# Performance work log

Measured on AMD Instinct MI355X. Metric: run time of the kernel, lower is better.

Reference implementation:

```python
import jax, jax.numpy as jnp
import numpy as np

N = 100000   # num nodes
E = 3200000  # num edges (avg degree 32)
EPS = 1e-5   # BatchNorm eps


def _gcn_norm(edge_index, edge_weight, n):
    # add self loops with weight 1 (PyG gcn_norm default fill_value=1.0)
    loops = jnp.arange(n, dtype=edge_index.dtype)
    ei = jnp.concatenate([edge_index, jnp.stack([loops, loops])], axis=1)
    ew = jnp.concatenate([edge_weight, jnp.ones((n,), edge_weight.dtype)])
    row, col = ei[0], ei[1]
    deg = jax.ops.segment_sum(ew, col, num_segments=n)
    deg_safe = jnp.where(deg > 0, deg, 1.0)
    dinv = jnp.where(deg > 0, jax.lax.rsqrt(deg_safe), 0.0)
    norm = dinv[row] * ew * dinv[col]  # [E+N]
    return row, col, norm


def _gcn_conv(x, row, col, norm, W, b, n):
    h = x @ W                                   # [N, out]
    msg = h[row] * norm[:, None]                # gather + scale, [E+N, out]
    out = jax.ops.segment_sum(msg, col, num_segments=n)  # scatter-add
    return out + b


def _bn(x, g, b, rm, rv):
    # BatchNorm1d in eval mode: running statistics
    return (x - rm) * jax.lax.rsqrt(rv + EPS) * g + b


def setup_inputs() -> dict:
    key = jax.random.key(0)
    ks = jax.random.split(key, 24)
    def p(i, shape, scale=1.0):
        return jax.random.normal(ks[i], shape, dtype=jnp.float32) * scale
    inp = {
        "x": p(0, (N, 1)),
        "edge_index": jax.random.randint(ks[1], (2, E), 0, N, dtype=jnp.int32),
        "edge_weight": jax.random.uniform(ks[2], (E,), dtype=jnp.float32),
        # GCNConv weights (glorot-ish scale) and biases
        "W1": p(3, (1, 16), 0.5), "b1": jnp.zeros((16,), jnp.float32),
        "W2": p(4, (16, 4), 0.25), "b2": jnp.zeros((4,), jnp.float32),
        "W3": p(5, (4, 1), 0.5), "b3": jnp.zeros((1,), jnp.float32),
        # BatchNorm params + running stats (running_var > 0)
        "g1": p(6, (16,), 0.1) + 1.0, "be1": p(7, (16,), 0.1),
        "rm1": p(8, (16,), 0.1), "rv1": jax.random.uniform(ks[9], (16,)) + 0.5,
        "g2": p(10, (4,), 0.1) + 1.0, "be2": p(11, (4,), 0.1),
        "rm2": p(12, (4,), 0.1), "rv2": jax.random.uniform(ks[13], (4,)) + 0.5,
        "g3": p(14, (1,), 0.1) + 1.0, "be3": p(15, (1,), 0.1),
        "rm3": p(16, (1,), 0.1), "rv3": jax.random.uniform(ks[17], (1,)) + 0.5,
        # end Linear(1, 1)
        "Wl": p(18, (1, 1)), "bl": p(19, (1,), 0.1),
    }
    return inp


def reference(x, edge_index, edge_weight,
              W1, b1, W2, b2, W3, b3,
              g1, be1, rm1, rv1,
              g2, be2, rm2, rv2,
              g3, be3, rm3, rv3,
              Wl, bl):
    row, col, norm = _gcn_norm(edge_index, edge_weight, N)
    h = _gcn_conv(x, row, col, norm, W1, b1, N)
    h = jax.nn.relu(_bn(h, g1, be1, rm1, rv1))  # dropout = identity in eval
    h = _gcn_conv(h, row, col, norm, W2, b2, N)
    h = jax.nn.relu(_bn(h, g2, be2, rm2, rv2))
    h = _gcn_conv(h, row, col, norm, W3, b3, N)
    h = _bn(h, g3, be3, rm3, rv3)
    h = h @ Wl + bl
    return jax.nn.sigmoid(h)
```

## Files before the change

### kernel.cpp

```cpp
#include <hip/hip_runtime.h>
#include <math.h>

#define NN 100000
#define NE 3200000
#define EPSBN 1e-5f

#define BSH 7
#define NB 782
#define NBLK 500
#define CHUNK 6400
#define C4 (CHUNK/4)
#define CAP 5120
#define BTA 512

#define NSB 12512
#define STCAP 4608

__device__ __forceinline__ float wave_allreduce(float a) {
    a += __shfl_xor(a, 1);  a += __shfl_xor(a, 2);  a += __shfl_xor(a, 4);
    a += __shfl_xor(a, 8);  a += __shfl_xor(a, 16); a += __shfl_xor(a, 32);
    return a;
}

__global__ void k_params_zero(const float* __restrict__ W1, const float* __restrict__ b1,
                              const float* __restrict__ g1, const float* __restrict__ be1,
                              const float* __restrict__ rm1, const float* __restrict__ rv1,
                              const float* __restrict__ b2,
                              const float* __restrict__ g2, const float* __restrict__ be2,
                              const float* __restrict__ rm2, const float* __restrict__ rv2,
                              const float* __restrict__ b3,
                              const float* __restrict__ g3, const float* __restrict__ be3,
                              const float* __restrict__ rm3, const float* __restrict__ rv3,
                              const float* __restrict__ Wl, const float* __restrict__ bl,
                              float* __restrict__ P, int* __restrict__ cnt) {
    int f = threadIdx.x;
    for (int i = f; i < NB; i += 1024) cnt[i] = 0;
    if (f < 16) {
        float k = g1[f] * rsqrtf(rv1[f] + EPSBN);
        P[f]      = W1[f] * k;
        P[16 + f] = (b1[f] - rm1[f]) * k + be1[f];
    }
    if (f < 4) {
        float k = g2[f] * rsqrtf(rv2[f] + EPSBN);
        P[32 + f] = k;
        P[36 + f] = (b2[f] - rm2[f]) * k + be2[f];
    }
    if (f == 0) {
        float k = g3[0] * rsqrtf(rv3[0] + EPSBN);
        P[40] = k * Wl[0];
        P[41] = ((b3[0] - rm3[0]) * k + be3[0]) * Wl[0] + bl[0];
    }
}

__global__ void k_build(const int* __restrict__ row, const int* __restrict__ col,
                        const float* __restrict__ ew, int* __restrict__ cnt,
                        uint2* __restrict__ rec) {
    __shared__ int h[NB];
    __shared__ int gb[NB];
    __shared__ int gsum[98];
    __shared__ uint2 st[CHUNK];
    __shared__ unsigned short sb[CHUNK];
    int blk = blockIdx.x, tid = threadIdx.x;
    for (int j = tid; j < NB; j += BTA) h[j] = 0;
    __syncthreads();

    const int4* c4 = (const int4*)(col + blk * CHUNK);
    int rk[4][4];
#pragma unroll
    for (int it = 0; it < 4; ++it) {
        int i = tid + it * BTA;
        if (i < C4) {
            int4 c = c4[i];
            rk[it][0] = atomicAdd(&h[c.x >> BSH], 1);
            rk[it][1] = atomicAdd(&h[c.y >> BSH], 1);
            rk[it][2] = atomicAdd(&h[c.z >> BSH], 1);
            rk[it][3] = atomicAdd(&h[c.w >> BSH], 1);
        }
    }
    __syncthreads();

    for (int j = tid; j < NB; j += BTA) {
        int hj = h[j];
        gb[j] = hj ? atomicAdd(&cnt[j], hj) : 0;
    }

    if (tid < 98) {
        int s = 0, b0 = tid * 8;
#pragma unroll
        for (int k = 0; k < 8; ++k) { int idx = b0 + k; s += (idx < NB) ? h[idx] : 0; }
        gsum[tid] = s;
    }
    __syncthreads();
    if (tid == 0) {
        int run = 0;
        for (int g = 0; g < 98; ++g) { int t = gsum[g]; gsum[g] = run; run += t; }
    }
    __syncthreads();
    if (tid < 98) {
        int run = gsum[tid], b0 = tid * 8;
#pragma unroll
        for (int k = 0; k < 8; ++k) {
            int idx = b0 + k;
            if (idx < NB) { int t = h[idx]; h[idx] = run; run += t; }
        }
    }
    __syncthreads();

    const int4*   r4 = (const int4*)(row + blk * CHUNK);
    const float4* w4 = (const float4*)(ew + blk * CHUNK);
#pragma unroll
    for (int it = 0; it < 4; ++it) {
        int i = tid + it * BTA;
        if (i < C4) {
            int4 c = c4[i]; int4 r = r4[i]; float4 w = w4[i];
            int b0 = c.x >> BSH, b1 = c.y >> BSH, b2 = c.z >> BSH, b3 = c.w >> BSH;
            int s0 = h[b0] + rk[it][0];
            st[s0] = make_uint2((unsigned)r.x | ((unsigned)(c.x & 127) << 17), __float_as_uint(w.x));
            sb[s0] = (unsigned short)b0;
            int s1 = h[b1] + rk[it][1];
            st[s1] = make_uint2((unsigned)r.y | ((unsigned)(c.y & 127) << 17), __float_as_uint(w.y));
            sb[s1] = (unsigned short)b1;
            int s2 = h[b2] + rk[it][2];
            st[s2] = make_uint2((unsigned)r.z | ((unsigned)(c.z & 127) << 17), __float_as_uint(w.z));
            sb[s2] = (unsigned short)b2;
            int s3 = h[b3] + rk[it][3];
            st[s3] = make_uint2((unsigned)r.w | ((unsigned)(c.w & 127) << 17), __float_as_uint(w.w));
            sb[s3] = (unsigned short)b3;
        }
    }
    __syncthreads();

    for (int i = tid; i < CHUNK; i += BTA) {
        int b = sb[i];
        rec[(size_t)b * CAP + gb[b] + (i - h[b])] = st[i];
    }
}

__global__ void k_subsort_deg(const int* __restrict__ cnt, uint2* __restrict__ rec,
                              int2* __restrict__ subsn, const float* __restrict__ x,
                              float* __restrict__ dinv, float* __restrict__ xd) {
    __shared__ uint2 st[STCAP];
    __shared__ int subtot[16];
    __shared__ int live[16];
    __shared__ int sstart[16];
    __shared__ int scount[16];
    int bin = blockIdx.x, tid = threadIdx.x;
    int lane = tid & 63, wv = tid >> 6;
    int n = cnt[bin];
    if (n > STCAP) n = STCAP;
    uint2* rb = rec + (size_t)bin * CAP;
    for (int i = tid; i < n; i += BTA) st[i] = rb[i];
    if (tid < 16) subtot[tid] = 0;
    __syncthreads();

    int myCnt = 0;
    for (int base = tid - lane; base < n; base += BTA) {
        int i = base + lane;
        bool v = (i < n);
        unsigned key = v ? ((st[i].x >> 20) & 15u) : 0u;
        unsigned long long bv = __ballot(v);
        unsigned long long q0 = __ballot(key & 1u);
        unsigned long long q1 = __ballot(key & 2u);
        unsigned long long q2 = __ballot(key & 4u);
        unsigned long long q3 = __ballot(key & 8u);
        if (lane < 16) {
            unsigned k = (unsigned)lane;
            unsigned long long m = bv;
            m &= (k & 1u) ? q0 : ~q0;
            m &= (k & 2u) ? q1 : ~q1;
            m &= (k & 4u) ? q2 : ~q2;
            m &= (k & 8u) ? q3 : ~q3;
            myCnt += __popcll(m);
        }
    }
    if (lane < 16 && myCnt) atomicAdd(&subtot[lane], myCnt);
    __syncthreads();

    if (tid == 0) {
        int run = 0;
        for (int k = 0; k < 16; ++k) {
            live[k] = run; sstart[k] = run; scount[k] = subtot[k];
            subsn[bin * 16 + k] = make_int2(bin * CAP + run, subtot[k]);
            run += subtot[k];
        }
    }
    __syncthreads();

    for (int base = tid - lane; base < n; base += BTA) {
        int i = base + lane;
        bool v = (i < n);
        uint2 rcd = v ? st[i] : make_uint2(0u, 0u);
        unsigned key = v ? ((rcd.x >> 20) & 15u) : 0u;
        unsigned long long bv = __ballot(v);
        unsigned long long q0 = __ballot(key & 1u);
        unsigned long long q1 = __ballot(key & 2u);
        unsigned long long q2 = __ballot(key & 4u);
        unsigned long long q3 = __ballot(key & 8u);
        int gb = 0;
        if (lane < 16) {
            unsigned k = (unsigned)lane;
            unsigned long long m = bv;
            m &= (k & 1u) ? q0 : ~q0;
            m &= (k & 2u) ? q1 : ~q1;
            m &= (k & 4u) ? q2 : ~q2;
            m &= (k & 8u) ? q3 : ~q3;
            int c = __popcll(m);
            if (c) gb = atomicAdd(&live[(int)k], c);
        }
        unsigned long long same = bv;
        same &= (key & 1u) ? q0 : ~q0;
        same &= (key & 2u) ? q1 : ~q1;
        same &= (key & 4u) ? q2 : ~q2;
        same &= (key & 8u) ? q3 : ~q3;
        unsigned long long below = (lane == 0) ? 0ull : ((~0ull) >> (64 - lane));
        int rank = __popcll(same & below);
        int mybase = __shfl(gb, (int)key);
        if (v) rb[mybase + rank] = rcd;
    }
    __syncthreads();

    for (int s = 0; s < 2; ++s) {
        int sbx = (wv << 1) | s;
        int n0 = scount[sbx];
        const uint2* p = rb + sstart[sbx];
        float acc[8] = {0.f, 0.f, 0.f, 0.f, 0.f, 0.f, 0.f, 0.f};
        for (int i = lane; i < n0; i += 64) {
            uint2 v = p[i];
            int cl = (v.x >> 17) & 7;
            float w = __uint_as_float(v.y);
#pragma unroll
            for (int c = 0; c < 8; ++c) acc[c] += (cl == c) ? w : 0.f;
        }
#pragma unroll
        for (int c = 0; c < 8; ++c) acc[c] = wave_allreduce(acc[c]);
        float mine = acc[0];
#pragma unroll
        for (int c = 1; c < 8; ++c) mine = (lane == c) ? acc[c] : mine;
        int colv = (bin << BSH) + (sbx << 3) + lane;
        if (lane < 8 && colv < NN) {
            float d = rsqrtf(1.0f + mine);
            dinv[colv] = d;
            xd[colv] = x[colv] * d;
        }
    }
}


__global__ void k_agg1_2(const int2* __restrict__ subsn, const uint2* __restrict__ rec,
                         const float* __restrict__ dinv, const float* __restrict__ xd,
                         const float* __restrict__ P, const float* __restrict__ W2,
                         float* __restrict__ m2s) {
    int tid = threadIdx.x, lane = tid & 63, wv = tid >> 6;
    int b = blockIdx.x * 8 + wv;
    int2 sn = subsn[b];
    float acc[8] = {0.f, 0.f, 0.f, 0.f, 0.f, 0.f, 0.f, 0.f};
    const uint2* p = rec + sn.x;
    int n0 = sn.y;
    int i = lane;
    for (; i + 64 < n0; i += 128) {
        uint2 v0 = p[i], v1 = p[i + 64];
        float g0 = xd[v0.x & 0x1FFFF] * __uint_as_float(v0.y);
        float g1 = xd[v1.x & 0x1FFFF] * __uint_as_float(v1.y);
        int c0 = (v0.x >> 17) & 7, c1 = (v1.x >> 17) & 7;
#pragma unroll
        for (int c = 0; c < 8; ++c) {
            acc[c] += (c0 == c) ? g0 : 0.f;
            acc[c] += (c1 == c) ? g1 : 0.f;
        }
    }
    for (; i < n0; i += 64) {
        uint2 v = p[i];
        int cl = (v.x >> 17) & 7;
        float g = xd[v.x & 0x1FFFF] * __uint_as_float(v.y);
#pragma unroll
        for (int c = 0; c < 8; ++c) acc[c] += (cl == c) ? g : 0.f;
    }
#pragma unroll
    for (int c = 0; c < 8; ++c) acc[c] = wave_allreduce(acc[c]);
    float mine = acc[0];
#pragma unroll
    for (int c = 1; c < 8; ++c) mine = (lane == c) ? acc[c] : mine;
    int colv = b * 8 + lane;
    if (lane < 8 && colv < NN) {
        float dc = dinv[colv];
        float y = (mine + xd[colv]) * dc;
        float m0 = 0.f, m1 = 0.f, m2v = 0.f, m3v = 0.f;
#pragma unroll
        for (int f = 0; f < 16; ++f) {
            float z = fmaxf(fmaf(y, P[f], P[16 + f]), 0.0f);
            m0 = fmaf(z, W2[f * 4 + 0], m0);
            m1 = fmaf(z, W2[f * 4 + 1], m1);
            m2v = fmaf(z, W2[f * 4 + 2], m2v);
            m3v = fmaf(z, W2[f * 4 + 3], m3v);
        }
        *(float4*)(m2s + 4 * colv) = make_float4(m0 * dc, m1 * dc, m2v * dc, m3v * dc);
    }
}

__global__ void k_agg2_2(const int2* __restrict__ subsn, const uint2* __restrict__ rec,
                         const float* __restrict__ dinv, const float* __restrict__ m2s,
                         const float* __restrict__ P, const float* __restrict__ W3,
                         float* __restrict__ m3s) {
    int tid = threadIdx.x, lane = tid & 63, wv = tid >> 6;
    int b = blockIdx.x * 8 + wv;
    int2 sn = subsn[b];
    float acc[8][4];
#pragma unroll
    for (int c = 0; c < 8; ++c)
#pragma unroll
        for (int j = 0; j < 4; ++j) acc[c][j] = 0.f;
    const uint2* p = rec + sn.x;
    int n0 = sn.y;
    int i = lane;
    for (; i + 64 < n0; i += 128) {
        uint2 v0 = p[i], v1 = p[i + 64];
        float w0 = __uint_as_float(v0.y), w1 = __uint_as_float(v1.y);
        float4 ma = *(const float4*)(m2s + 4 * (v0.x & 0x1FFFF));
        float4 mb = *(const float4*)(m2s + 4 * (v1.x & 0x1FFFF));
        int c0 = (v0.x >> 17) & 7, c1 = (v1.x >> 17) & 7;
#pragma unroll
        for (int c = 0; c < 8; ++c) {
            float s0 = (c0 == c) ? w0 : 0.f;
            float s1 = (c1 == c) ? w1 : 0.f;
            acc[c][0] = fmaf(ma.x, s0, fmaf(mb.x, s1, acc[c][0]));
            acc[c][1] = fmaf(ma.y, s0, fmaf(mb.y, s1, acc[c][1]));
            acc[c][2] = fmaf(ma.z, s0, fmaf(mb.z, s1, acc[c][2]));
            acc[c][3] = fmaf(ma.w, s0, fmaf(mb.w, s1, acc[c][3]));
        }
    }
    for (; i < n0; i += 64) {
        uint2 v = p[i];
        int cl = (v.x >> 17) & 7;
        float w = __uint_as_float(v.y);
        float4 m = *(const float4*)(m2s + 4 * (v.x & 0x1FFFF));
#pragma unroll
        for (int c = 0; c < 8; ++c) {
            float sel = (cl == c) ? w : 0.f;
            acc[c][0] = fmaf(m.x, sel, acc[c][0]);
            acc[c][1] = fmaf(m.y, sel, acc[c][1]);
            acc[c][2] = fmaf(m.z, sel, acc[c][2]);
            acc[c][3] = fmaf(m.w, sel, acc[c][3]);
        }
    }
#pragma unroll
    for (int c = 0; c < 8; ++c)
#pragma unroll
        for (int j = 0; j < 4; ++j) acc[c][j] = wave_allreduce(acc[c][j]);
    float r0 = acc[0][0], r1 = acc[0][1], r2 = acc[0][2], r3 = acc[0][3];
#pragma unroll
    for (int c = 1; c < 8; ++c) {
        r0 = (lane == c) ? acc[c][0] : r0;
        r1 = (lane == c) ? acc[c][1] : r1;
        r2 = (lane == c) ? acc[c][2] : r2;
        r3 = (lane == c) ? acc[c][3] : r3;
    }
    int colv = b * 8 + lane;
    if (lane < 8 && colv < NN) {
        float dc = dinv[colv];
        float4 mc = *(const float4*)(m2s + 4 * colv);
        float a0 = (r0 + mc.x) * dc;
        float a1 = (r1 + mc.y) * dc;
        float a2 = (r2 + mc.z) * dc;
        float a3 = (r3 + mc.w) * dc;
        float v3 = 0.f;
        v3 = fmaf(fmaxf(fmaf(a0, P[32], P[36]), 0.f), W3[0], v3);
        v3 = fmaf(fmaxf(fmaf(a1, P[33], P[37]), 0.f), W3[1], v3);
        v3 = fmaf(fmaxf(fmaf(a2, P[34], P[38]), 0.f), W3[2], v3);
        v3 = fmaf(fmaxf(fmaf(a3, P[35], P[39]), 0.f), W3[3], v3);
        m3s[colv] = v3 * dc;
    }
}

__global__ void k_agg3_2(const int2* __restrict__ subsn, const uint2* __restrict__ rec,
                         const float* __restrict__ dinv, const float* __restrict__ m3s,
                         const float* __restrict__ P, float* __restrict__ out) {
    int tid = threadIdx.x, lane = tid & 63, wv = tid >> 6;
    int b = blockIdx.x * 8 + wv;
    int2 sn = subsn[b];
    float acc[8] = {0.f, 0.f, 0.f, 0.f, 0.f, 0.f, 0.f, 0.f};
    const uint2* p = rec + sn.x;
    int n0 = sn.y;
    int i = lane;
    for (; i + 64 < n0; i += 128) {
        uint2 v0 = p[i], v1 = p[i + 64];
        float g0 = m3s[v0.x & 0x1FFFF] * __uint_as_float(v0.y);
        float g1 = m3s[v1.x & 0x1FFFF] * __uint_as_float(v1.y);
        int c0 = (v0.x >> 17) & 7, c1 = (v1.x >> 17) & 7;
#pragma unroll
        for (int c = 0; c < 8; ++c) {
            acc[c] += (c0 == c) ? g0 : 0.f;
            acc[c] += (c1 == c) ? g1 : 0.f;
        }
    }
    for (; i < n0; i += 64) {
        uint2 v = p[i];
        int cl = (v.x >> 17) & 7;
        float g = m3s[v.x & 0x1FFFF] * __uint_as_float(v.y);
#pragma unroll
        for (int c = 0; c < 8; ++c) acc[c] += (cl == c) ? g : 0.f;
    }
#pragma unroll
    for (int c = 0; c < 8; ++c) acc[c] = wave_allreduce(acc[c]);
    float mine = acc[0];
#pragma unroll
    for (int c = 1; c < 8; ++c) mine = (lane == c) ? acc[c] : mine;
    int colv = b * 8 + lane;
    if (lane < 8 && colv < NN) {
        float t = fmaf((mine + m3s[colv]) * dinv[colv], P[40], P[41]);
        out[colv] = 1.0f / (1.0f + __expf(-t));
    }
}


__global__ void k_init_deg(float* __restrict__ deg) {
    int i = blockIdx.x * blockDim.x + threadIdx.x;
    if (i < NN) deg[i] = 1.0f;
}

__global__ void k_dinv_y1(const float* __restrict__ deg, const float* __restrict__ x,
                          float* __restrict__ dinv, float* __restrict__ y1) {
    int i = blockIdx.x * blockDim.x + threadIdx.x;
    if (i >= NN) return;
    float d = rsqrtf(deg[i]);
    dinv[i] = d;
    y1[i] = x[i] * d * d;
}

__global__ void k_l1_epi(const float* __restrict__ y1, const float* __restrict__ dinv,
                         const float* __restrict__ P, const float* __restrict__ W2,
                         float* __restrict__ m2, float* __restrict__ agg2) {
    int i = blockIdx.x * blockDim.x + threadIdx.x;
    if (i >= NN) return;
    float y = y1[i];
    float m0 = 0.f, m1 = 0.f, m2v = 0.f, m3v = 0.f;
#pragma unroll
    for (int f = 0; f < 16; ++f) {
        float z = fmaxf(fmaf(y, P[f], P[16 + f]), 0.0f);
        m0 = fmaf(z, W2[f * 4 + 0], m0);
        m1 = fmaf(z, W2[f * 4 + 1], m1);
        m2v = fmaf(z, W2[f * 4 + 2], m2v);
        m3v = fmaf(z, W2[f * 4 + 3], m3v);
    }
    float d = dinv[i];
    float d2 = d * d;
    *(float4*)(m2 + 4 * i)   = make_float4(m0, m1, m2v, m3v);
    *(float4*)(agg2 + 4 * i) = make_float4(m0 * d2, m1 * d2, m2v * d2, m3v * d2);
}

__global__ void k_l2_epi(const float* __restrict__ agg2, const float* __restrict__ dinv,
                         const float* __restrict__ P, const float* __restrict__ W3,
                         float* __restrict__ m3, float* __restrict__ agg3) {
    int i = blockIdx.x * blockDim.x + threadIdx.x;
    if (i >= NN) return;
    float4 a = *(const float4*)(agg2 + 4 * i);
    float v = 0.f;
    v = fmaf(fmaxf(fmaf(a.x, P[32], P[36]), 0.f), W3[0], v);
    v = fmaf(fmaxf(fmaf(a.y, P[33], P[37]), 0.f), W3[1], v);
    v = fmaf(fmaxf(fmaf(a.z, P[34], P[38]), 0.f), W3[2], v);
    v = fmaf(fmaxf(fmaf(a.w, P[35], P[39]), 0.f), W3[3], v);
    float d = dinv[i];
    m3[i] = v;
    agg3[i] = v * d * d;
}

__global__ void k_final(const float* __restrict__ agg3, const float* __restrict__ P,
                        float* __restrict__ out) {
    int i = blockIdx.x * blockDim.x + threadIdx.x;
    if (i >= NN) return;
    float t = fmaf(agg3[i], P[40], P[41]);
    out[i] = 1.0f / (1.0f + __expf(-t));
}

__global__ void k_deg(const int* __restrict__ col, const float* __restrict__ ew,
                      float* __restrict__ deg) {
    int e = (blockIdx.x * blockDim.x + threadIdx.x) * 4;
    if (e >= NE) return;
    int4 c = *(const int4*)(col + e);
    float4 w = *(const float4*)(ew + e);
    atomicAdd(&deg[c.x], w.x);
    atomicAdd(&deg[c.y], w.y);
    atomicAdd(&deg[c.z], w.z);
    atomicAdd(&deg[c.w], w.w);
}

__global__ void k_norm_agg1(const int* __restrict__ row, const int* __restrict__ col,
                            const float* __restrict__ ew, const float* __restrict__ dinv,
                            const float* __restrict__ x,
                            float* __restrict__ norm, float* __restrict__ y1) {
    int e = (blockIdx.x * blockDim.x + threadIdx.x) * 4;
    if (e >= NE) return;
    int4 r = *(const int4*)(row + e);
    int4 c = *(const int4*)(col + e);
    float4 w = *(const float4*)(ew + e);
    float4 nv;
    nv.x = dinv[r.x] * w.x * dinv[c.x];
    nv.y = dinv[r.y] * w.y * dinv[c.y];
    nv.z = dinv[r.z] * w.z * dinv[c.z];
    nv.w = dinv[r.w] * w.w * dinv[c.w];
    *(float4*)(norm + e) = nv;
    atomicAdd(&y1[c.x], x[r.x] * nv.x);
    atomicAdd(&y1[c.y], x[r.y] * nv.y);
    atomicAdd(&y1[c.z], x[r.z] * nv.z);
    atomicAdd(&y1[c.w], x[r.w] * nv.w);
}

__global__ void k_agg2(const int* __restrict__ row, const int* __restrict__ col,
                       const float* __restrict__ norm, const float* __restrict__ m2,
                       float* __restrict__ agg2) {
    int e = blockIdx.x * blockDim.x + threadIdx.x;
    if (e >= NE) return;
    int r = row[e], c = col[e];
    float nv = norm[e];
    float4 m = *(const float4*)(m2 + 4 * r);
    atomicAdd(&agg2[4 * c + 0], m.x * nv);
    atomicAdd(&agg2[4 * c + 1], m.y * nv);
    atomicAdd(&agg2[4 * c + 2], m.z * nv);
    atomicAdd(&agg2[4 * c + 3], m.w * nv);
}

__global__ void k_agg3(const int* __restrict__ row, const int* __restrict__ col,
                       const float* __restrict__ norm, const float* __restrict__ m3,
                       float* __restrict__ agg3) {
    int e = (blockIdx.x * blockDim.x + threadIdx.x) * 4;
    if (e >= NE) return;
    int4 r = *(const int4*)(row + e);
    int4 c = *(const int4*)(col + e);
    float4 nv = *(const float4*)(norm + e);
    atomicAdd(&agg3[c.x], m3[r.x] * nv.x);
    atomicAdd(&agg3[c.y], m3[r.y] * nv.y);
    atomicAdd(&agg3[c.z], m3[r.z] * nv.z);
    atomicAdd(&agg3[c.w], m3[r.w] * nv.w);
}


extern "C" void kernel_launch(void* const* d_in, const int* in_sizes, int n_in,
                              void* d_out, int out_size, void* d_ws, size_t ws_size,
                              hipStream_t stream) {
    const float* x  = (const float*)d_in[0];
    const int*   ei = (const int*)d_in[1];
    const float* ew = (const float*)d_in[2];
    const float* W1 = (const float*)d_in[3];
    const float* b1 = (const float*)d_in[4];
    const float* W2 = (const float*)d_in[5];
    const float* b2 = (const float*)d_in[6];
    const float* W3 = (const float*)d_in[7];
    const float* b3 = (const float*)d_in[8];
    const float* g1 = (const float*)d_in[9];
    const float* be1 = (const float*)d_in[10];
    const float* rm1 = (const float*)d_in[11];
    const float* rv1 = (const float*)d_in[12];
    const float* g2 = (const float*)d_in[13];
    const float* be2 = (const float*)d_in[14];
    const float* rm2 = (const float*)d_in[15];
    const float* rv2 = (const float*)d_in[16];
    const float* g3 = (const float*)d_in[17];
    const float* be3 = (const float*)d_in[18];
    const float* rm3 = (const float*)d_in[19];
    const float* rv3 = (const float*)d_in[20];
    const float* Wl = (const float*)d_in[21];
    const float* bl = (const float*)d_in[22];
    float* out = (float*)d_out;

    const int* row = ei;
    const int* col = ei + NE;

    const int BT = 256;
    const int gN = (NN + BT - 1) / BT;
    const int gE4 = (NE / 4 + BT - 1) / BT;

    char* ws = (char*)d_ws;

    if (ws_size >= 37000000u) {
        float* P     = (float*)(ws);
        int*   cnt   = (int*)  (ws + 4096);
        int2*  subsn = (int2*) (ws + 16384);
        float* dinv  = (float*)(ws + 524288);
        float* xd    = (float*)(ws + 1048576);
        float* m3s   = (float*)(ws + 1572864);
        float* m2s   = (float*)(ws + 2097152);
        uint2* rec   = (uint2*)(ws + 4194304);

        k_params_zero<<<1, 1024, 0, stream>>>(W1, b1, g1, be1, rm1, rv1,
                                              b2, g2, be2, rm2, rv2,
                                              b3, g3, be3, rm3, rv3, Wl, bl, P, cnt);
        k_build<<<NBLK, BTA, 0, stream>>>(row, col, ew, cnt, rec);
        k_subsort_deg<<<NB, BTA, 0, stream>>>(cnt, rec, subsn, x, dinv, xd);
        k_agg1_2<<<NSB / 8, BTA, 0, stream>>>(subsn, rec, dinv, xd, P, W2, m2s);
        k_agg2_2<<<NSB / 8, BTA, 0, stream>>>(subsn, rec, dinv, m2s, P, W3, m3s);
        k_agg3_2<<<NSB / 8, BTA, 0, stream>>>(subsn, rec, dinv, m3s, P, out);
    } else {
        float* deg   = (float*)(ws);
        float* dinv  = (float*)(ws + 400000);
        float* y1    = (float*)(ws + 800000);
        float* m2    = (float*)(ws + 1200000);
        float* agg2  = (float*)(ws + 2800000);
        float* m3    = (float*)(ws + 4400000);
        float* agg3  = (float*)(ws + 4800000);
        float* Pf    = (float*)(ws + 5200000);
        float* norm  = (float*)(ws + 5200256);
        const int gE1 = (NE + BT - 1) / BT;

        k_params_zero<<<1, 1024, 0, stream>>>(W1, b1, g1, be1, rm1, rv1,
                                              b2, g2, be2, rm2, rv2,
                                              b3, g3, be3, rm3, rv3, Wl, bl, Pf, (int*)(ws + 5300000));
        k_init_deg<<<gN, BT, 0, stream>>>(deg);
        k_deg<<<gE4, BT, 0, stream>>>(col, ew, deg);
        k_dinv_y1<<<gN, BT, 0, stream>>>(deg, x, dinv, y1);
        k_norm_agg1<<<gE4, BT, 0, stream>>>(row, col, ew, dinv, x, norm, y1);
        k_l1_epi<<<gN, BT, 0, stream>>>(y1, dinv, Pf, W2, m2, agg2);
        k_agg2<<<gE1, BT, 0, stream>>>(row, col, norm, m2, agg2);
        k_l2_epi<<<gN, BT, 0, stream>>>(agg2, dinv, Pf, W3, m3, agg3);
        k_agg3<<<gE4, BT, 0, stream>>>(row, col, norm, m3, agg3);
        k_final<<<gN, BT, 0, stream>>>(agg3, Pf, out);
    }
}
```

Before: 134.6 us.

## Fully sort edges by column and aggregate with one thread per column

The subsort kernel now sorts records by the full 7-bit in-bin column key, staging records in registers and writing the sorted order through shared memory. It emits a per-column start/count table. The three aggregation kernels switch from wave-per-8-columns with select-accumulate and wave allreduces to one thread per column looping over its contiguous edge segment. This removes redundant select ALU work and shuffle reductions, at the cost of uncoalesced per-thread record reads and possible load imbalance across columns.

```diff
diff --git a/kernel.cpp b/kernel.cpp
--- a/kernel.cpp
+++ b/kernel.cpp
@@ -13,8 +13,8 @@
 #define CAP 5120
 #define BTA 512
 
-#define NSB 12512
 #define STCAP 4608
+#define NCOL 100096
 
 __device__ __forceinline__ float wave_allreduce(float a) {
     a += __shfl_xor(a, 1);  a += __shfl_xor(a, 2);  a += __shfl_xor(a, 4);
@@ -137,11 +137,12 @@
 }
 
 __global__ void k_subsort_deg(const int* __restrict__ cnt, uint2* __restrict__ rec,
-                              int2* __restrict__ subsn, const float* __restrict__ x,
+                              int2* __restrict__ colsc, const float* __restrict__ x,
                               float* __restrict__ dinv, float* __restrict__ xd) {
     __shared__ uint2 st[STCAP];
-    __shared__ int subtot[16];
-    __shared__ int live[16];
+    __shared__ int subtot[128];
+    __shared__ int colbase[128];
+    __shared__ int live[128];
     __shared__ int sstart[16];
     __shared__ int scount[16];
     int bin = blockIdx.x, tid = threadIdx.x;
@@ -149,80 +150,109 @@
     int n = cnt[bin];
     if (n > STCAP) n = STCAP;
     uint2* rb = rec + (size_t)bin * CAP;
-    for (int i = tid; i < n; i += BTA) st[i] = rb[i];
-    if (tid < 16) subtot[tid] = 0;
-    __syncthreads();
-
-    int myCnt = 0;
-    for (int base = tid - lane; base < n; base += BTA) {
-        int i = base + lane;
+
+    uint2 r[9];
+#pragma unroll
+    for (int k = 0; k < 9; ++k) {
+        int i = tid + k * BTA;
+        if (i < n) r[k] = rb[i];
+    }
+    if (tid < 128) subtot[tid] = 0;
+    __syncthreads();
+
+    int c0acc = 0, c1acc = 0;
+#pragma unroll
+    for (int k = 0; k < 9; ++k) {
+        int i = tid + k * BTA;
         bool v = (i < n);
-        unsigned key = v ? ((st[i].x >> 20) & 15u) : 0u;
+        unsigned key = v ? ((r[k].x >> 17) & 127u) : 0u;
         unsigned long long bv = __ballot(v);
         unsigned long long q0 = __ballot(key & 1u);
         unsigned long long q1 = __ballot(key & 2u);
         unsigned long long q2 = __ballot(key & 4u);
         unsigned long long q3 = __ballot(key & 8u);
-        if (lane < 16) {
-            unsigned k = (unsigned)lane;
-            unsigned long long m = bv;
-            m &= (k & 1u) ? q0 : ~q0;
-            m &= (k & 2u) ? q1 : ~q1;
-            m &= (k & 4u) ? q2 : ~q2;
-            m &= (k & 8u) ? q3 : ~q3;
-            myCnt += __popcll(m);
-        }
-    }
-    if (lane < 16 && myCnt) atomicAdd(&subtot[lane], myCnt);
+        unsigned long long q4 = __ballot(key & 16u);
+        unsigned long long q5 = __ballot(key & 32u);
+        unsigned long long q6 = __ballot(key & 64u);
+        unsigned long long m5 = bv;
+        m5 &= (lane & 1)  ? q0 : ~q0;
+        m5 &= (lane & 2)  ? q1 : ~q1;
+        m5 &= (lane & 4)  ? q2 : ~q2;
+        m5 &= (lane & 8)  ? q3 : ~q3;
+        m5 &= (lane & 16) ? q4 : ~q4;
+        m5 &= (lane & 32) ? q5 : ~q5;
+        c0acc += __popcll(m5 & ~q6);
+        c1acc += __popcll(m5 & q6);
+    }
+    if (c0acc) atomicAdd(&subtot[lane], c0acc);
+    if (c1acc) atomicAdd(&subtot[lane + 64], c1acc);
     __syncthreads();
 
     if (tid == 0) {
         int run = 0;
-        for (int k = 0; k < 16; ++k) {
-            live[k] = run; sstart[k] = run; scount[k] = subtot[k];
-            subsn[bin * 16 + k] = make_int2(bin * CAP + run, subtot[k]);
+        for (int k = 0; k < 128; ++k) {
+            colbase[k] = run; live[k] = run;
             run += subtot[k];
         }
-    }
-    __syncthreads();
-
-    for (int base = tid - lane; base < n; base += BTA) {
-        int i = base + lane;
+        for (int s = 0; s < 16; ++s) {
+            sstart[s] = colbase[s * 8];
+            int e = (s == 15) ? n : colbase[s * 8 + 8];
+            scount[s] = e - sstart[s];
+        }
+    }
+    __syncthreads();
+
+    if (tid < 128)
+        colsc[bin * 128 + tid] = make_int2(bin * CAP + colbase[tid], subtot[tid]);
+
+#pragma unroll
+    for (int k = 0; k < 9; ++k) {
+        int i = tid + k * BTA;
         bool v = (i < n);
-        uint2 rcd = v ? st[i] : make_uint2(0u, 0u);
-        unsigned key = v ? ((rcd.x >> 20) & 15u) : 0u;
+        uint2 rcd = v ? r[k] : make_uint2(0u, 0u);
+        unsigned key = v ? ((rcd.x >> 17) & 127u) : 0u;
         unsigned long long bv = __ballot(v);
         unsigned long long q0 = __ballot(key & 1u);
         unsigned long long q1 = __ballot(key & 2u);
         unsigned long long q2 = __ballot(key & 4u);
         unsigned long long q3 = __ballot(key & 8u);
-        int gb = 0;
-        if (lane < 16) {
-            unsigned k = (unsigned)lane;
-            unsigned long long m = bv;
-            m &= (k & 1u) ? q0 : ~q0;
-            m &= (k & 2u) ? q1 : ~q1;
-            m &= (k & 4u) ? q2 : ~q2;
-            m &= (k & 8u) ? q3 : ~q3;
-            int c = __popcll(m);
-            if (c) gb = atomicAdd(&live[(int)k], c);
-        }
+        unsigned long long q4 = __ballot(key & 16u);
+        unsigned long long q5 = __ballot(key & 32u);
+        unsigned long long q6 = __ballot(key & 64u);
+        unsigned long long m5 = bv;
+        m5 &= (lane & 1)  ? q0 : ~q0;
+        m5 &= (lane & 2)  ? q1 : ~q1;
+        m5 &= (lane & 4)  ? q2 : ~q2;
+        m5 &= (lane & 8)  ? q3 : ~q3;
+        m5 &= (lane & 16) ? q4 : ~q4;
+        m5 &= (lane & 32) ? q5 : ~q5;
+        int cc0 = __popcll(m5 & ~q6);
+        int cc1 = __popcll(m5 & q6);
+        int gb0 = cc0 ? atomicAdd(&live[lane], cc0) : 0;
+        int gb1 = cc1 ? atomicAdd(&live[lane + 64], cc1) : 0;
         unsigned long long same = bv;
-        same &= (key & 1u) ? q0 : ~q0;
-        same &= (key & 2u) ? q1 : ~q1;
-        same &= (key & 4u) ? q2 : ~q2;
-        same &= (key & 8u) ? q3 : ~q3;
+        same &= (key & 1u)  ? q0 : ~q0;
+        same &= (key & 2u)  ? q1 : ~q1;
+        same &= (key & 4u)  ? q2 : ~q2;
+        same &= (key & 8u)  ? q3 : ~q3;
+        same &= (key & 16u) ? q4 : ~q4;
+        same &= (key & 32u) ? q5 : ~q5;
+        same &= (key & 64u) ? q6 : ~q6;
         unsigned long long below = (lane == 0) ? 0ull : ((~0ull) >> (64 - lane));
         int rank = __popcll(same & below);
-        int mybase = __shfl(gb, (int)key);
-        if (v) rb[mybase + rank] = rcd;
-    }
-    __syncthreads();
+        int s0 = __shfl(gb0, (int)(key & 63u));
+        int s1 = __shfl(gb1, (int)(key & 63u));
+        int mybase = (key & 64u) ? s1 : s0;
+        if (v) st[mybase + rank] = rcd;
+    }
+    __syncthreads();
+
+    for (int i = tid; i < n; i += BTA) rb[i] = st[i];
 
     for (int s = 0; s < 2; ++s) {
         int sbx = (wv << 1) | s;
         int n0 = scount[sbx];
-        const uint2* p = rb + sstart[sbx];
+        const uint2* p = &st[sstart[sbx]];
         float acc[8] = {0.f, 0.f, 0.f, 0.f, 0.f, 0.f, 0.f, 0.f};
         for (int i = lane; i < n0; i += 64) {
             uint2 v = p[i];
@@ -246,169 +276,98 @@
 }
 
 
-__global__ void k_agg1_2(const int2* __restrict__ subsn, const uint2* __restrict__ rec,
+__global__ void k_agg1_c(const int2* __restrict__ colsc, const uint2* __restrict__ rec,
                          const float* __restrict__ dinv, const float* __restrict__ xd,
                          const float* __restrict__ P, const float* __restrict__ W2,
                          float* __restrict__ m2s) {
-    int tid = threadIdx.x, lane = tid & 63, wv = tid >> 6;
-    int b = blockIdx.x * 8 + wv;
-    int2 sn = subsn[b];
-    float acc[8] = {0.f, 0.f, 0.f, 0.f, 0.f, 0.f, 0.f, 0.f};
-    const uint2* p = rec + sn.x;
-    int n0 = sn.y;
-    int i = lane;
-    for (; i + 64 < n0; i += 128) {
-        uint2 v0 = p[i], v1 = p[i + 64];
+    int col = blockIdx.x * blockDim.x + threadIdx.x;
+    if (col >= NN) return;
+    int2 sc = colsc[col];
+    const uint2* p = rec + sc.x;
+    float a = 0.f;
+    int i = 0;
+    for (; i + 1 < sc.y; i += 2) {
+        uint2 v0 = p[i], v1 = p[i + 1];
         float g0 = xd[v0.x & 0x1FFFF] * __uint_as_float(v0.y);
         float g1 = xd[v1.x & 0x1FFFF] * __uint_as_float(v1.y);
-        int c0 = (v0.x >> 17) & 7, c1 = (v1.x >> 17) & 7;
-#pragma unroll
-        for (int c = 0; c < 8; ++c) {
-            acc[c] += (c0 == c) ? g0 : 0.f;
-            acc[c] += (c1 == c) ? g1 : 0.f;
-        }
-    }
-    for (; i < n0; i += 64) {
-        uint2 v = p[i];
-        int cl = (v.x >> 17) & 7;
-        float g = xd[v.x & 0x1FFFF] * __uint_as_float(v.y);
-#pragma unroll
-        for (int c = 0; c < 8; ++c) acc[c] += (cl == c) ? g : 0.f;
-    }
-#pragma unroll
-    for (int c = 0; c < 8; ++c) acc[c] = wave_allreduce(acc[c]);
-    float mine = acc[0];
-#pragma unroll
-    for (int c = 1; c < 8; ++c) mine = (lane == c) ? acc[c] : mine;
-    int colv = b * 8 + lane;
-    if (lane < 8 && colv < NN) {
-        float dc = dinv[colv];
-        float y = (mine + xd[colv]) * dc;
-        float m0 = 0.f, m1 = 0.f, m2v = 0.f, m3v = 0.f;
-#pragma unroll
-        for (int f = 0; f < 16; ++f) {
-            float z = fmaxf(fmaf(y, P[f], P[16 + f]), 0.0f);
-            m0 = fmaf(z, W2[f * 4 + 0], m0);
-            m1 = fmaf(z, W2[f * 4 + 1], m1);
-            m2v = fmaf(z, W2[f * 4 + 2], m2v);
-            m3v = fmaf(z, W2[f * 4 + 3], m3v);
-        }
-        *(float4*)(m2s + 4 * colv) = make_float4(m0 * dc, m1 * dc, m2v * dc, m3v * dc);
-    }
-}
-
-__global__ void k_agg2_2(const int2* __restrict__ subsn, const uint2* __restrict__ rec,
+        a += g0 + g1;
+    }
+    if (i < sc.y) { uint2 v = p[i]; a += xd[v.x & 0x1FFFF] * __uint_as_float(v.y); }
+    float dc = dinv[col];
+    float y = (a + xd[col]) * dc;
+    float m0 = 0.f, m1 = 0.f, m2v = 0.f, m3v = 0.f;
+#pragma unroll
+    for (int f = 0; f < 16; ++f) {
+        float z = fmaxf(fmaf(y, P[f], P[16 + f]), 0.0f);
+        m0 = fmaf(z, W2[f * 4 + 0], m0);
+        m1 = fmaf(z, W2[f * 4 + 1], m1);
+        m2v = fmaf(z, W2[f * 4 + 2], m2v);
+        m3v = fmaf(z, W2[f * 4 + 3], m3v);
+    }
+    *(float4*)(m2s + 4 * col) = make_float4(m0 * dc, m1 * dc, m2v * dc, m3v * dc);
+}
+
+__global__ void k_agg2_c(const int2* __restrict__ colsc, const uint2* __restrict__ rec,
                          const float* __restrict__ dinv, const float* __restrict__ m2s,
                          const float* __restrict__ P, const float* __restrict__ W3,
                          float* __restrict__ m3s) {
-    int tid = threadIdx.x, lane = tid & 63, wv = tid >> 6;
-    int b = blockIdx.x * 8 + wv;
-    int2 sn = subsn[b];
-    float acc[8][4];
-#pragma unroll
-    for (int c = 0; c < 8; ++c)
-#pragma unroll
-        for (int j = 0; j < 4; ++j) acc[c][j] = 0.f;
-    const uint2* p = rec + sn.x;
-    int n0 = sn.y;
-    int i = lane;
-    for (; i + 64 < n0; i += 128) {
-        uint2 v0 = p[i], v1 = p[i + 64];
+    int col = blockIdx.x * blockDim.x + threadIdx.x;
+    if (col >= NN) return;
+    int2 sc = colsc[col];
+    const uint2* p = rec + sc.x;
+    float a0 = 0.f, a1 = 0.f, a2 = 0.f, a3 = 0.f;
+    int i = 0;
+    for (; i + 1 < sc.y; i += 2) {
+        uint2 v0 = p[i], v1 = p[i + 1];
         float w0 = __uint_as_float(v0.y), w1 = __uint_as_float(v1.y);
         float4 ma = *(const float4*)(m2s + 4 * (v0.x & 0x1FFFF));
         float4 mb = *(const float4*)(m2s + 4 * (v1.x & 0x1FFFF));
-        int c0 = (v0.x >> 17) & 7, c1 = (v1.x >> 17) & 7;
-#pragma unroll
-        for (int c = 0; c < 8; ++c) {
-            float s0 = (c0 == c) ? w0 : 0.f;
-            float s1 = (c1 == c) ? w1 : 0.f;
-            acc[c][0] = fmaf(ma.x, s0, fmaf(mb.x, s1, acc[c][0]));
-            acc[c][1] = fmaf(ma.y, s0, fmaf(mb.y, s1, acc[c][1]));
-            acc[c][2] = fmaf(ma.z, s0, fmaf(mb.z, s1, acc[c][2]));
-            acc[c][3] = fmaf(ma.w, s0, fmaf(mb.w, s1, acc[c][3]));
-        }
-    }
-    for (; i < n0; i += 64) {
+        a0 = fmaf(ma.x, w0, fmaf(mb.x, w1, a0));
+        a1 = fmaf(ma.y, w0, fmaf(mb.y, w1, a1));
+        a2 = fmaf(ma.z, w0, fmaf(mb.z, w1, a2));
+        a3 = fmaf(ma.w, w0, fmaf(mb.w, w1, a3));
+    }
+    if (i < sc.y) {
         uint2 v = p[i];
-        int cl = (v.x >> 17) & 7;
         float w = __uint_as_float(v.y);
         float4 m = *(const float4*)(m2s + 4 * (v.x & 0x1FFFF));
-#pragma unroll
-        for (int c = 0; c < 8; ++c) {
-            float sel = (cl == c) ? w : 0.f;
-            acc[c][0] = fmaf(m.x, sel, acc[c][0]);
-            acc[c][1] = fmaf(m.y, sel, acc[c][1]);
-            acc[c][2] = fmaf(m.z, sel, acc[c][2]);
-            acc[c][3] = fmaf(m.w, sel, acc[c][3]);
-        }
-    }
-#pragma unroll
-    for (int c = 0; c < 8; ++c)
-#pragma unroll
-        for (int j = 0; j < 4; ++j) acc[c][j] = wave_allreduce(acc[c][j]);
-    float r0 = acc[0][0], r1 = acc[0][1], r2 = acc[0][2], r3 = acc[0][3];
-#pragma unroll
-    for (int c = 1; c < 8; ++c) {
-        r0 = (lane == c) ? acc[c][0] : r0;
-        r1 = (lane == c) ? acc[c][1] : r1;
-        r2 = (lane == c) ? acc[c][2] : r2;
-        r3 = (lane == c) ? acc[c][3] : r3;
-    }
-    int colv = b * 8 + lane;
-    if (lane < 8 && colv < NN) {
-        float dc = dinv[colv];
-        float4 mc = *(const float4*)(m2s + 4 * colv);
-        float a0 = (r0 + mc.x) * dc;
-        float a1 = (r1 + mc.y) * dc;
-        float a2 = (r2 + mc.z) * dc;
-        float a3 = (r3 + mc.w) * dc;
-        float v3 = 0.f;
-        v3 = fmaf(fmaxf(fmaf(a0, P[32], P[36]), 0.f), W3[0], v3);
-        v3 = fmaf(fmaxf(fmaf(a1, P[33], P[37]), 0.f), W3[1], v3);
-        v3 = fmaf(fmaxf(fmaf(a2, P[34], P[38]), 0.f), W3[2], v3);
-        v3 = fmaf(fmaxf(fmaf(a3, P[35], P[39]), 0.f), W3[3], v3);
-        m3s[colv] = v3 * dc;
-    }
-}
-
-__global__ void k_agg3_2(const int2* __restrict__ subsn, const uint2* __restrict__ rec,
+        a0 = fmaf(m.x, w, a0);
+        a1 = fmaf(m.y, w, a1);
+        a2 = fmaf(m.z, w, a2);
+        a3 = fmaf(m.w, w, a3);
+    }
+    float dc = dinv[col];
+    float4 mc = *(const float4*)(m2s + 4 * col);
+    float b0 = (a0 + mc.x) * dc;
+    float b1 = (a1 + mc.y) * dc;
+    float b2 = (a2 + mc.z) * dc;
+    float b3 = (a3 + mc.w) * dc;
+    float v3 = 0.f;
+    v3 = fmaf(fmaxf(fmaf(b0, P[32], P[36]), 0.f), W3[0], v3);
+    v3 = fmaf(fmaxf(fmaf(b1, P[33], P[37]), 0.f), W3[1], v3);
+    v3 = fmaf(fmaxf(fmaf(b2, P[34], P[38]), 0.f), W3[2], v3);
+    v3 = fmaf(fmaxf(fmaf(b3, P[35], P[39]), 0.f), W3[3], v3);
+    m3s[col] = v3 * dc;
+}
+
+__global__ void k_agg3_c(const int2* __restrict__ colsc, const uint2* __restrict__ rec,
                          const float* __restrict__ dinv, const float* __restrict__ m3s,
                          const float* __restrict__ P, float* __restrict__ out) {
-    int tid = threadIdx.x, lane = tid & 63, wv = tid >> 6;
-    int b = blockIdx.x * 8 + wv;
-    int2 sn = subsn[b];
-    float acc[8] = {0.f, 0.f, 0.f, 0.f, 0.f, 0.f, 0.f, 0.f};
-    const uint2* p = rec + sn.x;
-    int n0 = sn.y;
-    int i = lane;
-    for (; i + 64 < n0; i += 128) {
-        uint2 v0 = p[i], v1 = p[i + 64];
+    int col = blockIdx.x * blockDim.x + threadIdx.x;
+    if (col >= NN) return;
+    int2 sc = colsc[col];
+    const uint2* p = rec + sc.x;
+    float a = 0.f;
+    int i = 0;
+    for (; i + 1 < sc.y; i += 2) {
+        uint2 v0 = p[i], v1 = p[i + 1];
         float g0 = m3s[v0.x & 0x1FFFF] * __uint_as_float(v0.y);
         float g1 = m3s[v1.x & 0x1FFFF] * __uint_as_float(v1.y);
-        int c0 = (v0.x >> 17) & 7, c1 = (v1.x >> 17) & 7;
-#pragma unroll
-        for (int c = 0; c < 8; ++c) {
-            acc[c] += (c0 == c) ? g0 : 0.f;
-            acc[c] += (c1 == c) ? g1 : 0.f;
-        }
-    }
-    for (; i < n0; i += 64) {
-        uint2 v = p[i];
-        int cl = (v.x >> 17) & 7;
-        float g = m3s[v.x & 0x1FFFF] * __uint_as_float(v.y);
-#pragma unroll
-        for (int c = 0; c < 8; ++c) acc[c] += (cl == c) ? g : 0.f;
-    }
-#pragma unroll
-    for (int c = 0; c < 8; ++c) acc[c] = wave_allreduce(acc[c]);
-    float mine = acc[0];
-#pragma unroll
-    for (int c = 1; c < 8; ++c) mine = (lane == c) ? acc[c] : mine;
-    int colv = b * 8 + lane;
-    if (lane < 8 && colv < NN) {
-        float t = fmaf((mine + m3s[colv]) * dinv[colv], P[40], P[41]);
-        out[colv] = 1.0f / (1.0f + __expf(-t));
-    }
+        a += g0 + g1;
+    }
+    if (i < sc.y) { uint2 v = p[i]; a += m3s[v.x & 0x1FFFF] * __uint_as_float(v.y); }
+    float t = fmaf((a + m3s[col]) * dinv[col], P[40], P[41]);
+    out[col] = 1.0f / (1.0f + __expf(-t));
 }
 
 
@@ -567,27 +526,28 @@
     const int BT = 256;
     const int gN = (NN + BT - 1) / BT;
     const int gE4 = (NE / 4 + BT - 1) / BT;
+    const int gC = (NN + BT - 1) / BT;
 
     char* ws = (char*)d_ws;
 
-    if (ws_size >= 37000000u) {
+    if (ws_size >= 36800000u) {
         float* P     = (float*)(ws);
         int*   cnt   = (int*)  (ws + 4096);
-        int2*  subsn = (int2*) (ws + 16384);
-        float* dinv  = (float*)(ws + 524288);
-        float* xd    = (float*)(ws + 1048576);
-        float* m3s   = (float*)(ws + 1572864);
-        float* m2s   = (float*)(ws + 2097152);
-        uint2* rec   = (uint2*)(ws + 4194304);
+        int2*  colsc = (int2*) (ws + 16384);
+        float* dinv  = (float*)(ws + 1048576);
+        float* xd    = (float*)(ws + 1572864);
+        float* m3s   = (float*)(ws + 2097152);
+        float* m2s   = (float*)(ws + 2621440);
+        uint2* rec   = (uint2*)(ws + 4718592);
 
         k_params_zero<<<1, 1024, 0, stream>>>(W1, b1, g1, be1, rm1, rv1,
                                               b2, g2, be2, rm2, rv2,
                                               b3, g3, be3, rm3, rv3, Wl, bl, P, cnt);
         k_build<<<NBLK, BTA, 0, stream>>>(row, col, ew, cnt, rec);
-        k_subsort_deg<<<NB, BTA, 0, stream>>>(cnt, rec, subsn, x, dinv, xd);
-        k_agg1_2<<<NSB / 8, BTA, 0, stream>>>(subsn, rec, dinv, xd, P, W2, m2s);
-        k_agg2_2<<<NSB / 8, BTA, 0, stream>>>(subsn, rec, dinv, m2s, P, W3, m3s);
-        k_agg3_2<<<NSB / 8, BTA, 0, stream>>>(subsn, rec, dinv, m3s, P, out);
+        k_subsort_deg<<<NB, BTA, 0, stream>>>(cnt, rec, colsc, x, dinv, xd);
+        k_agg1_c<<<gC, BT, 0, stream>>>(colsc, rec, dinv, xd, P, W2, m2s);
+        k_agg2_c<<<gC, BT, 0, stream>>>(colsc, rec, dinv, m2s, P, W3, m3s);
+        k_agg3_c<<<gC, BT, 0, stream>>>(colsc, rec, dinv, m3s, P, out);
     } else {
         float* deg   = (float*)(ws);
         float* dinv  = (float*)(ws + 400000);
```

New measurement: 150.8 us. +12.0%, slower.
